# Kernel tuning notes

Measured on AMD Instinct MI355X. Metric: run time of the kernel, lower is better.

## Reference

```python
import jax, jax.numpy as jnp
import numpy as np

NUM_FEATURES = 50


def _build_port_feature_mask(num_node_features: int = NUM_FEATURES) -> np.ndarray:
    """(F, 6) mask: port p has track if any connect/port-revenue feature for p is nonzero."""
    mask = np.zeros((num_node_features, 6), dtype=np.float32)
    feat_idx = 23
    for i in range(6):
        for j in range(i):
            mask[feat_idx, i] = 1.0
            mask[feat_idx, j] = 1.0
            feat_idx += 1
    for i in range(6):
        for k in range(2):
            mask[38 + i * 2 + k, i] = 1.0
    return mask


def setup_inputs() -> dict:
    key = jax.random.key(0)
    k1, k2 = jax.random.split(key)
    B, N, F = 16, 1024, NUM_FEATURES
    node_features = jax.random.normal(k1, (B, N, F), dtype=jnp.float32)
    direction_matrix = jax.random.randint(k2, (N, N), 0, 7, dtype=jnp.int32)
    port_feature_mask = jnp.asarray(_build_port_feature_mask(F))
    return {
        "node_features": node_features,
        "direction_matrix": direction_matrix,
        "port_feature_mask": port_feature_mask,
    }


def reference(node_features, direction_matrix, port_feature_mask):
    B, N, _ = node_features.shape
    # (B, N, 6): per-hex, per-port track indicator
    port_activity = node_features @ port_feature_mask
    port_has_track = (port_activity > 0).astype(node_features.dtype)

    dir_mat = direction_matrix.astype(jnp.int32)
    adj_mask = (dir_mat != 6).astype(node_features.dtype)  # (N, N)
    dir_clamped = jnp.minimum(dir_mat, 5)                  # (N, N)
    opp_clamped = jnp.minimum((dir_mat + 3) % 6, 5)        # (N, N)

    i_idx = jnp.arange(N)[:, None]  # row index i, broadcasts with (N, N)
    j_idx = jnp.arange(N)[None, :]  # col index j
    # src[b, i, j] = port_has_track[b, i, dir_clamped[i, j]]
    src_ports = port_has_track[:, i_idx, dir_clamped]  # (B, N, N)
    # dst[b, i, j] = port_has_track[b, j, opp_clamped[i, j]]
    dst_ports = port_has_track[:, j_idx, opp_clamped]  # (B, N, N)

    return src_ports * dst_ports * adj_mask[None, :, :]
```

## Files before the change

### kernel.cpp

```cpp
#include <hip/hip_runtime.h>

#define N_NODES 1024
#define B_SZ 16
#define F_SZ 50

typedef float f32x4 __attribute__((ext_vector_type(4)));

__global__ __launch_bounds__(64) void ports_kernel(
        const float* __restrict__ nf,
        unsigned char* __restrict__ bits) {
    int idx = blockIdx.x * 64 + threadIdx.x;
    const float* r = nf + (size_t)idx * F_SZ;

    float f[27];
    #pragma unroll
    for (int q = 0; q < 27; ++q) f[q] = r[23 + q];

    float a0 = (((((f[0]  + f[1])  + f[3])  + f[6])  + f[10]) + f[15]) + f[16];
    float a1 = (((((f[0]  + f[2])  + f[4])  + f[7])  + f[11]) + f[17]) + f[18];
    float a2 = (((((f[1]  + f[2])  + f[5])  + f[8])  + f[12]) + f[19]) + f[20];
    float a3 = (((((f[3]  + f[4])  + f[5])  + f[9])  + f[13]) + f[21]) + f[22];
    float a4 = (((((f[6]  + f[7])  + f[8])  + f[9])  + f[14]) + f[23]) + f[24];
    float a5 = (((((f[10] + f[11]) + f[12]) + f[13]) + f[14]) + f[25]) + f[26];

    unsigned m = 0;
    m |= (a0 > 0.0f) ? 1u  : 0u;
    m |= (a1 > 0.0f) ? 2u  : 0u;
    m |= (a2 > 0.0f) ? 4u  : 0u;
    m |= (a3 > 0.0f) ? 8u  : 0u;
    m |= (a4 > 0.0f) ? 16u : 0u;
    m |= (a5 > 0.0f) ? 32u : 0u;
    bits[idx] = (unsigned char)m;
}

__global__ __launch_bounds__(256) void connect_kernel(
        const int* __restrict__ dir,
        const unsigned char* __restrict__ bits,
        float* __restrict__ out) {
    const int q = blockIdx.x;
    const int t = threadIdx.x;
    const int p0 = q * 4;
    const int b = p0 >> 10;

    uchar4 dv4 = ((const uchar4*)(bits + b * N_NODES))[t];
    unsigned tb[4] = {dv4.x, dv4.y, dv4.z, dv4.w};

    #pragma unroll
    for (int r = 0; r < 4; ++r) {
        const int p = p0 + r;
        const int i = p & (N_NODES - 1);

        int4 d = ((const int4*)(dir + (size_t)i * N_NODES))[t];
        int dvv[4] = {d.x, d.y, d.z, d.w};
        unsigned s = bits[b * N_NODES + i];

        f32x4 o;
        #pragma unroll
        for (int k = 0; k < 4; ++k) {
            int dval = dvv[k];
            unsigned am = (dval != 6) ? 1u : 0u;
            unsigned ds = (unsigned)min(dval, 5);
            unsigned os = (unsigned)min((dval + 3) % 6, 5);
            o[k] = ((s >> ds) & (tb[k] >> os) & am & 1u) ? 1.0f : 0.0f;
        }
        __builtin_nontemporal_store(
            o, (f32x4*)(out + (size_t)p * N_NODES) + t);
    }
}

extern "C" void kernel_launch(void* const* d_in, const int* in_sizes, int n_in,
                              void* d_out, int out_size, void* d_ws, size_t ws_size,
                              hipStream_t stream) {
    const float* nf  = (const float*)d_in[0];
    const int*   dir = (const int*)d_in[1];
    float* out = (float*)d_out;
    unsigned char* bits = (unsigned char*)d_ws;

    ports_kernel<<<(B_SZ * N_NODES) / 64, 64, 0, stream>>>(nf, bits);
    connect_kernel<<<(B_SZ * N_NODES) / 4, 256, 0, stream>>>(dir, bits, out);
}
```

Before: 21.10 us.

## Fuse port-bit computation into connect kernel with shared-memory bits

```diff
diff --git a/kernel.cpp b/kernel.cpp
--- a/kernel.cpp
+++ b/kernel.cpp
@@ -3,56 +3,58 @@
 #define N_NODES 1024
 #define B_SZ 16
 #define F_SZ 50
+#define ROWS_PER_BLK 32
 
 typedef float f32x4 __attribute__((ext_vector_type(4)));
 
-__global__ __launch_bounds__(64) void ports_kernel(
+__global__ __launch_bounds__(256) void fused_kernel(
         const float* __restrict__ nf,
-        unsigned char* __restrict__ bits) {
-    int idx = blockIdx.x * 64 + threadIdx.x;
-    const float* r = nf + (size_t)idx * F_SZ;
+        const int* __restrict__ dir,
+        float* __restrict__ out) {
+    __shared__ unsigned char sbits[N_NODES];
 
-    float f[27];
-    #pragma unroll
-    for (int q = 0; q < 27; ++q) f[q] = r[23 + q];
-
-    float a0 = (((((f[0]  + f[1])  + f[3])  + f[6])  + f[10]) + f[15]) + f[16];
-    float a1 = (((((f[0]  + f[2])  + f[4])  + f[7])  + f[11]) + f[17]) + f[18];
-    float a2 = (((((f[1]  + f[2])  + f[5])  + f[8])  + f[12]) + f[19]) + f[20];
-    float a3 = (((((f[3]  + f[4])  + f[5])  + f[9])  + f[13]) + f[21]) + f[22];
-    float a4 = (((((f[6]  + f[7])  + f[8])  + f[9])  + f[14]) + f[23]) + f[24];
-    float a5 = (((((f[10] + f[11]) + f[12]) + f[13]) + f[14]) + f[25]) + f[26];
-
-    unsigned m = 0;
-    m |= (a0 > 0.0f) ? 1u  : 0u;
-    m |= (a1 > 0.0f) ? 2u  : 0u;
-    m |= (a2 > 0.0f) ? 4u  : 0u;
-    m |= (a3 > 0.0f) ? 8u  : 0u;
-    m |= (a4 > 0.0f) ? 16u : 0u;
-    m |= (a5 > 0.0f) ? 32u : 0u;
-    bits[idx] = (unsigned char)m;
-}
-
-__global__ __launch_bounds__(256) void connect_kernel(
-        const int* __restrict__ dir,
-        const unsigned char* __restrict__ bits,
-        float* __restrict__ out) {
     const int q = blockIdx.x;
     const int t = threadIdx.x;
-    const int p0 = q * 4;
-    const int b = p0 >> 10;
+    const int b = q >> 5;
+    const int rowbase = (q & 31) * ROWS_PER_BLK;
 
-    uchar4 dv4 = ((const uchar4*)(bits + b * N_NODES))[t];
+    #pragma unroll
+    for (int c = 0; c < 4; ++c) {
+        const int n = t + 256 * c;
+        const float* r = nf + ((size_t)b * N_NODES + n) * F_SZ;
+        float f[27];
+        #pragma unroll
+        for (int x = 0; x < 27; ++x) f[x] = r[23 + x];
+
+        float a0 = (((((f[0]  + f[1])  + f[3])  + f[6])  + f[10]) + f[15]) + f[16];
+        float a1 = (((((f[0]  + f[2])  + f[4])  + f[7])  + f[11]) + f[17]) + f[18];
+        float a2 = (((((f[1]  + f[2])  + f[5])  + f[8])  + f[12]) + f[19]) + f[20];
+        float a3 = (((((f[3]  + f[4])  + f[5])  + f[9])  + f[13]) + f[21]) + f[22];
+        float a4 = (((((f[6]  + f[7])  + f[8])  + f[9])  + f[14]) + f[23]) + f[24];
+        float a5 = (((((f[10] + f[11]) + f[12]) + f[13]) + f[14]) + f[25]) + f[26];
+
+        unsigned m = 0;
+        m |= (a0 > 0.0f) ? 1u  : 0u;
+        m |= (a1 > 0.0f) ? 2u  : 0u;
+        m |= (a2 > 0.0f) ? 4u  : 0u;
+        m |= (a3 > 0.0f) ? 8u  : 0u;
+        m |= (a4 > 0.0f) ? 16u : 0u;
+        m |= (a5 > 0.0f) ? 32u : 0u;
+        sbits[n] = (unsigned char)m;
+    }
+    __syncthreads();
+
+    uchar4 dv4 = *(const uchar4*)&sbits[t * 4];
     unsigned tb[4] = {dv4.x, dv4.y, dv4.z, dv4.w};
 
-    #pragma unroll
-    for (int r = 0; r < 4; ++r) {
-        const int p = p0 + r;
-        const int i = p & (N_NODES - 1);
+    const size_t obase = ((size_t)b * N_NODES + rowbase) * N_NODES;
+    #pragma unroll 4
+    for (int r = 0; r < ROWS_PER_BLK; ++r) {
+        const int i = rowbase + r;
+        const unsigned s = sbits[i];
 
         int4 d = ((const int4*)(dir + (size_t)i * N_NODES))[t];
         int dvv[4] = {d.x, d.y, d.z, d.w};
-        unsigned s = bits[b * N_NODES + i];
 
         f32x4 o;
         #pragma unroll
@@ -63,8 +65,7 @@
             unsigned os = (unsigned)min((dval + 3) % 6, 5);
             o[k] = ((s >> ds) & (tb[k] >> os) & am & 1u) ? 1.0f : 0.0f;
         }
-        __builtin_nontemporal_store(
-            o, (f32x4*)(out + (size_t)p * N_NODES) + t);
+        *((f32x4*)(out + obase + (size_t)r * N_NODES) + t) = o;
     }
 }
 
@@ -74,8 +75,6 @@
     const float* nf  = (const float*)d_in[0];
     const int*   dir = (const int*)d_in[1];
     float* out = (float*)d_out;
-    unsigned char* bits = (unsigned char*)d_ws;
 
-    ports_kernel<<<(B_SZ * N_NODES) / 64, 64, 0, stream>>>(nf, bits);
-    connect_kernel<<<(B_SZ * N_NODES) / 4, 256, 0, stream>>>(dir, bits, out);
+    fused_kernel<<<(B_SZ * N_NODES) / ROWS_PER_BLK, 256, 0, stream>>>(nf, dir, out);
 }
```

New measurement: 25.74 us. 1.22x slower.
